# Kernel optimization log

Hardware: AMD Instinct MI355X
Metric: run time of the kernel (lower is better)

The kernel has to match this reference:

```python
import jax, jax.numpy as jnp
import numpy as np

EMBED_DIM = 768
NUM_HEADS = 12
HEAD_DIM = EMBED_DIM // NUM_HEADS
SCALE = HEAD_DIM ** -0.5
B, N = 8, 1024


def setup_inputs() -> dict:
    key = jax.random.key(0)
    ks = jax.random.split(key, 5)
    return {
        "x": jax.random.normal(ks[0], (B, N, EMBED_DIM), dtype=jnp.float32),
        "qkv_w": jax.random.normal(ks[1], (3 * EMBED_DIM, EMBED_DIM), dtype=jnp.float32) * 0.02,
        "qkv_b": jax.random.normal(ks[2], (3 * EMBED_DIM,), dtype=jnp.float32) * 0.02,
        "proj_w": jax.random.normal(ks[3], (EMBED_DIM, EMBED_DIM), dtype=jnp.float32) * 0.02,
        "proj_b": jax.random.normal(ks[4], (EMBED_DIM,), dtype=jnp.float32) * 0.02,
    }


def reference(x, qkv_w, qkv_b, proj_w, proj_b):
    b, n, c = x.shape
    h, hd = NUM_HEADS, HEAD_DIM
    # QKV projection: [b,n,3c]
    qkv = jnp.einsum("bnc,dc->bnd", x, qkv_w) + qkv_b
    qkv = qkv.reshape(b, n, 3, h, hd).transpose(2, 0, 3, 1, 4)  # [3,b,h,n,hd]
    q, k, v = qkv[0], qkv[1], qkv[2]
    # scaled dot-product attention (eager path; dropout is identity in eval)
    attn = jnp.einsum("bhqd,bhkd->bhqk", q, k) * SCALE
    attn = jax.nn.softmax(attn, axis=-1)
    out = jnp.einsum("bhqk,bhkd->bhqd", attn, v)  # [b,h,n,hd]
    out = out.transpose(0, 2, 1, 3).reshape(b, n, c)
    # output projection
    return jnp.einsum("bnc,dc->bnd", out, proj_w) + proj_b
```

## Files before the change

### kernel.cpp

```cpp
#include <hip/hip_runtime.h>
#include <hip/hip_bf16.h>

typedef __attribute__((ext_vector_type(4))) float f32x4;
typedef __attribute__((ext_vector_type(16))) float f32x16;
typedef __attribute__((ext_vector_type(8))) short short8;
typedef unsigned short u16;

#define MFMA(a, b, c) __builtin_amdgcn_mfma_f32_16x16x32_bf16((a), (b), (c), 0, 0, 0)
#define MFMA32(a, b, c) __builtin_amdgcn_mfma_f32_32x32x16_bf16((a), (b), (c), 0, 0, 0)

#define WAITVM_BAR(N) do {                                          \
    asm volatile("s_waitcnt vmcnt(" #N ")" ::: "memory");           \
    __builtin_amdgcn_s_barrier();                                   \
    __builtin_amdgcn_sched_barrier(0);                              \
} while (0)
#define BAR2() do {                                                 \
    __builtin_amdgcn_sched_barrier(0);                              \
    __builtin_amdgcn_s_barrier();                                   \
    __builtin_amdgcn_sched_barrier(0);                              \
} while (0)

static constexpr int EMBED = 768;
static constexpr int NH = 12;
static constexpr int HD = 64;
static constexpr int BATCH = 8;
static constexpr int SEQ = 1024;

__device__ __forceinline__ u16 f2bu(float f) {
    __hip_bfloat16 h = __float2bfloat16(f);
    u16 u; __builtin_memcpy(&u, &h, 2); return u;
}
__device__ __forceinline__ float exp2a(float x) {
    float r; asm("v_exp_f32 %0, %1" : "=v"(r) : "v"(x)); return r;
}
__device__ __forceinline__ unsigned cvt_pk_bf16(float lo, float hi) {
    unsigned r; asm("v_cvt_pk_bf16_f32 %0, %1, %2" : "=v"(r) : "v"(lo), "v"(hi)); return r;
}
__device__ __forceinline__ float max3f(float a, float b, float c) {
    return fmaxf(fmaxf(a, b), c);
}
__device__ __forceinline__ void swap32(unsigned& a, unsigned& b) {
    asm volatile("v_permlane32_swap_b32 %0, %1" : "+v"(a), "+v"(b));
}
__device__ __forceinline__ short8 mk8(unsigned w0, unsigned w1, unsigned w2, unsigned w3) {
    union { unsigned u[4]; short8 s; } c;
    c.u[0] = w0; c.u[1] = w1; c.u[2] = w2; c.u[3] = w3;
    return c.s;
}

__global__ void cvt_all_k(const float* __restrict__ x, const float* __restrict__ w1,
                          const float* __restrict__ w2,
                          u16* __restrict__ xb, u16* __restrict__ wb, u16* __restrict__ pw) {
    const int n1 = BATCH * SEQ * EMBED;
    const int n2 = 3 * EMBED * EMBED;
    const int n3 = EMBED * EMBED;
    int i = (blockIdx.x * blockDim.x + threadIdx.x) * 4;
    const float* src; u16* dst;
    if (i < n1)            { src = x  + i;             dst = xb + i; }
    else if (i < n1 + n2)  { src = w1 + (i - n1);      dst = wb + (i - n1); }
    else if (i < n1+n2+n3) { src = w2 + (i - n1 - n2); dst = pw + (i - n1 - n2); }
    else return;
    float4 v = *reinterpret_cast<const float4*>(src);
    ushort4 o;
    o.x = f2bu(v.x); o.y = f2bu(v.y); o.z = f2bu(v.z); o.w = f2bu(v.w);
    *reinterpret_cast<ushort4*>(dst) = o;
}

template <int EPI>
__global__ __launch_bounds__(256)
void gemm_bt_k(const u16* __restrict__ A, const u16* __restrict__ Bw,
               const float* __restrict__ bias,
               u16* __restrict__ q_out, u16* __restrict__ k_out,
               u16* __restrict__ vt_out, float* __restrict__ f_out)
{
    __shared__ __attribute__((aligned(16))) char smem[65536];
    const int tid  = threadIdx.x;
    const int wave = tid >> 6, lane = tid & 63;
    const int hi   = lane >> 4, l15 = lane & 15;
    const int wr   = wave >> 1, wc = wave & 1;
    const int bm   = blockIdx.x, bn = blockIdx.y;

    f32x4 acc[4][4] = {};

    const size_t arow0 = (size_t)bm * 128;
    const size_t brow0 = (size_t)bn * 128;

    auto stage = [&](int buf, int kt) {
        char* Ab = smem + buf * 32768;
        char* Bb = Ab + 16384;
#pragma unroll
        for (int c = 0; c < 4; ++c) {
            int ck   = c * 4 + wave;
            int p    = ck * 1024 + lane * 16;
            int row  = p >> 7;
            int pcol = (p & 127) ^ ((row & 7) << 4);
            const u16* srcA = A  + (arow0 + row) * EMBED + kt + (pcol >> 1);
            const u16* srcB = Bw + (brow0 + row) * EMBED + kt + (pcol >> 1);
            __builtin_amdgcn_global_load_lds((const __attribute__((address_space(1))) void*)srcA,
                                             (__attribute__((address_space(3))) void*)(Ab + ck * 1024), 16, 0, 0);
            __builtin_amdgcn_global_load_lds((const __attribute__((address_space(1))) void*)srcB,
                                             (__attribute__((address_space(3))) void*)(Bb + ck * 1024), 16, 0, 0);
        }
    };

    const int sw_l = (l15 & 7) << 4;
    int aoff[2], boff[2];
#pragma unroll
    for (int kk = 0; kk < 2; ++kk) {
        int col = (kk * 64 + hi * 16) ^ sw_l;
        aoff[kk] = (wr * 64 + l15) * 128 + col;
        boff[kk] = (wc * 64 + l15) * 128 + col;
    }

    auto comp = [&](int buf) {
#pragma unroll
        for (int kk = 0; kk < 2; ++kk) {
            short8 af[4], bf[4];
#pragma unroll
            for (int mi = 0; mi < 4; ++mi)
                af[mi] = *reinterpret_cast<const short8*>(smem + buf * 32768 + aoff[kk] + mi * 2048);
#pragma unroll
            for (int ni = 0; ni < 4; ++ni)
                bf[ni] = *reinterpret_cast<const short8*>(smem + buf * 32768 + 16384 + boff[kk] + ni * 2048);
#pragma unroll
            for (int mi = 0; mi < 4; ++mi)
#pragma unroll
                for (int ni = 0; ni < 4; ++ni)
                    acc[mi][ni] = MFMA(af[mi], bf[ni], acc[mi][ni]);
        }
    };

    stage(0, 0);
#pragma unroll
    for (int tt = 0; tt < 5; ++tt) {
        stage(1, (2 * tt + 1) * 64);
        WAITVM_BAR(8);
        comp(0);
        BAR2();
        stage(0, (2 * tt + 2) * 64);
        WAITVM_BAR(8);
        comp(1);
        BAR2();
    }
    stage(1, 11 * 64);
    WAITVM_BAR(8);
    comp(0);
    BAR2();
    WAITVM_BAR(0);
    comp(1);

#pragma unroll
    for (int mi = 0; mi < 4; ++mi) {
        int crow0 = bm * 128 + wr * 64 + mi * 16 + hi * 4;
#pragma unroll
        for (int ni = 0; ni < 4; ++ni) {
            int ccol = bn * 128 + wc * 64 + ni * 16 + l15;
            float bv = bias[ccol];
            if constexpr (EPI == 0) {
                int which = ccol / 768;
                int rem   = ccol - which * 768;
                int hh = rem >> 6, hd = rem & 63;
                int bb = crow0 >> 10, nn0 = crow0 & 1023;
                size_t bh = (size_t)(bb * NH + hh);
                if (which == 2) {
                    uint2 pk;
                    pk.x = cvt_pk_bf16(acc[mi][ni][0] + bv, acc[mi][ni][1] + bv);
                    pk.y = cvt_pk_bf16(acc[mi][ni][2] + bv, acc[mi][ni][3] + bv);
                    *reinterpret_cast<uint2*>(&vt_out[(bh * HD + hd) * SEQ + nn0]) = pk;
                } else if (which == 0) {
#pragma unroll
                    for (int r = 0; r < 4; ++r)
                        q_out[(bh * SEQ + nn0 + r) * HD + hd] =
                            f2bu((acc[mi][ni][r] + bv) * 0.18033688f);
                } else {
#pragma unroll
                    for (int r = 0; r < 4; ++r)
                        k_out[(bh * SEQ + nn0 + r) * HD + hd] = f2bu(acc[mi][ni][r] + bv);
                }
            } else {
#pragma unroll
                for (int r = 0; r < 4; ++r)
                    f_out[(size_t)(crow0 + r) * EMBED + ccol] = acc[mi][ni][r] + bv;
            }
        }
    }
}

__global__ __launch_bounds__(256, 3)
void attn_k(const u16* __restrict__ Q, const u16* __restrict__ K,
            const u16* __restrict__ Vt, u16* __restrict__ AO)
{
    __shared__ __attribute__((aligned(16))) u16 kv[3][8192];

    const int tid = threadIdx.x;
    const int w   = tid >> 6, lane = tid & 63;
    const int h   = lane >> 5, l31 = lane & 31;
    const int f   = blockIdx.x;
    const int xcd = f & 7, i = f >> 3;
    const int bh  = xcd * 12 + (i % 12);
    const int q0w = (i / 12) * 128 + w * 32;

    const u16* Qh = Q  + (size_t)bh * SEQ * HD;
    const u16* Kh = K  + (size_t)bh * SEQ * HD;
    const u16* Vh = Vt + (size_t)bh * HD * SEQ;

    short8 qf[4];
#pragma unroll
    for (int ds = 0; ds < 4; ++ds)
        qf[ds] = *reinterpret_cast<const short8*>(
            Qh + (size_t)(q0w + l31) * HD + ds * 16 + h * 8);
    __builtin_amdgcn_sched_barrier(0);

    const u16* sptr[4]; int doff[4]; int sadv[4];
#pragma unroll
    for (int c = 0; c < 4; ++c) {
        int ch = c * 4 + w;
        int mc = ch & 7;
        int p  = mc * 1024 + lane * 16;
        int row = p >> 7;
        int colb = (p & 127) ^ ((row & 7) << 4);
        if (ch < 8) { sptr[c] = Kh + (size_t)row * HD + (colb >> 1); sadv[c] = 64 * HD; doff[c] = mc * 512; }
        else        { sptr[c] = Vh + (size_t)row * SEQ + (colb >> 1); sadv[c] = 64;     doff[c] = 4096 + mc * 512; }
    }
    auto stage = [&](int buf, int t) {
#pragma unroll
        for (int c = 0; c < 4; ++c)
            __builtin_amdgcn_global_load_lds(
                (const __attribute__((address_space(1))) void*)(sptr[c] + (size_t)t * sadv[c]),
                (__attribute__((address_space(3))) void*)(&kv[buf][doff[c]]), 16, 0, 0);
    };

    stage(0, 0);
    stage(1, 1);

    const int sw_l = (l31 & 7) << 4;
    int koff[4];
#pragma unroll
    for (int ds = 0; ds < 4; ++ds)
        koff[ds] = l31 * 128 + ((ds * 32 + h * 16) ^ sw_l);

    union { unsigned u[4]; short8 s; } oc;
    oc.u[0] = oc.u[1] = oc.u[2] = oc.u[3] = 0x3F803F80u;
    const short8 ones8 = oc.s;

    f32x16 accO[2] = {};
    f32x16 lsum = {};
    float m = 8.f;

    auto tile = [&](int BC) {
        const char* base = (const char*)kv + BC * 16384;
        f32x16 st[2] = {{0}, {0}};
        __builtin_amdgcn_s_setprio(1);
#pragma unroll
        for (int mf = 0; mf < 2; ++mf)
#pragma unroll
            for (int ds = 0; ds < 4; ++ds) {
                short8 kf = *reinterpret_cast<const short8*>(base + mf * 4096 + koff[ds]);
                st[mf] = MFMA32(kf, qf[ds], st[mf]);
            }
        __builtin_amdgcn_s_setprio(0);

        float x0 = max3f(st[0][0],  st[0][1],  st[0][2]);
        float x1 = max3f(st[0][3],  st[0][4],  st[0][5]);
        float x2 = max3f(st[0][6],  st[0][7],  st[0][8]);
        float x3 = max3f(st[0][9],  st[0][10], st[0][11]);
        float x4 = max3f(st[0][12], st[0][13], st[0][14]);
        float x5 = max3f(st[0][15], st[1][0],  st[1][1]);
        float x6 = max3f(st[1][2],  st[1][3],  st[1][4]);
        float x7 = max3f(st[1][5],  st[1][6],  st[1][7]);
        float x8 = max3f(st[1][8],  st[1][9],  st[1][10]);
        float x9 = max3f(st[1][11], st[1][12], st[1][13]);
        float xa = fmaxf(st[1][14], st[1][15]);
        float tm = fmaxf(max3f(max3f(x0, x1, x2), max3f(x3, x4, x5), max3f(x6, x7, x8)),
                         max3f(x9, xa, -1e30f));
        tm = fmaxf(tm, __shfl_xor(tm, 32, 64));

        unsigned pkw[2][8];
#pragma unroll
        for (int mf = 0; mf < 2; ++mf)
#pragma unroll
            for (int p = 0; p < 8; ++p) {
                float e0 = exp2a(st[mf][2 * p]     - m);
                float e1 = exp2a(st[mf][2 * p + 1] - m);
                pkw[mf][p] = cvt_pk_bf16(e0, e1);
            }

        short8 pb[4];
#pragma unroll
        for (int ks = 0; ks < 4; ++ks) {
            int mf = ks >> 1, b4 = (ks & 1) * 4;
            unsigned E0 = pkw[mf][b4 + 0], E1 = pkw[mf][b4 + 1];
            unsigned D0 = pkw[mf][b4 + 2], D1 = pkw[mf][b4 + 3];
            swap32(E0, D0);
            swap32(E1, D1);
            pb[ks] = mk8(E0, E1, D0, D1);
        }

        __builtin_amdgcn_s_setprio(1);
#pragma unroll
        for (int ks = 0; ks < 4; ++ks)
            lsum = MFMA32(ones8, pb[ks], lsum);
#pragma unroll
        for (int df = 0; df < 2; ++df)
#pragma unroll
            for (int ks = 0; ks < 4; ++ks) {
                short8 vf = *reinterpret_cast<const short8*>(base + 8192 + df * 4096 + koff[ks]);
                accO[df] = MFMA32(vf, pb[ks], accO[df]);
            }
        __builtin_amdgcn_s_setprio(0);

        if (!__all(tm <= m + 8.f)) {
            float mn = fmaxf(m, tm);
            float s  = exp2a(m - mn);
            m = mn;
#pragma unroll
            for (int r = 0; r < 16; ++r) {
                accO[0][r] *= s; accO[1][r] *= s; lsum[r] *= s;
            }
        }
    };

    auto one = [&](int bc, int bs, int tn, bool ds) {
        asm volatile("s_waitcnt vmcnt(4)" ::: "memory");
        __builtin_amdgcn_s_barrier();
        __builtin_amdgcn_sched_barrier(0);
        if (ds) stage(bs, tn);
        tile(bc);
        __builtin_amdgcn_sched_barrier(0);
    };

    one(0, 2, 2, true);
    one(1, 0, 3, true);
    one(2, 1, 4, true);
    for (int g = 1; g < 5; ++g) {
        one(0, 2, 3 * g + 2, true);
        one(1, 0, 3 * g + 3, 3 * g + 3 <= 15);
        one(2, 1, 3 * g + 4, 3 * g + 4 <= 15);
    }
    asm volatile("s_waitcnt vmcnt(0)" ::: "memory");
    __builtin_amdgcn_s_barrier();
    __builtin_amdgcn_sched_barrier(0);
    tile(0);

    float linv = 1.f / lsum[0];
    const int bb = bh / NH, hh = bh - bb * NH;
    size_t rowb = ((size_t)bb * SEQ + q0w + l31) * EMBED + hh * HD;
#pragma unroll
    for (int df = 0; df < 2; ++df)
#pragma unroll
        for (int g = 0; g < 4; ++g) {
            float o0 = accO[df][4 * g + 0] * linv;
            float o1 = accO[df][4 * g + 1] * linv;
            float o2 = accO[df][4 * g + 2] * linv;
            float o3 = accO[df][4 * g + 3] * linv;
            uint2 pk;
            pk.x = cvt_pk_bf16(o0, o1);
            pk.y = cvt_pk_bf16(o2, o3);
            *reinterpret_cast<uint2*>(&AO[rowb + df * 32 + 8 * g + 4 * h]) = pk;
        }
}

extern "C" void kernel_launch(void* const* d_in, const int* in_sizes, int n_in,
                              void* d_out, int out_size, void* d_ws, size_t ws_size,
                              hipStream_t stream)
{
    const float* x      = (const float*)d_in[0];
    const float* qkv_w  = (const float*)d_in[1];
    const float* qkv_b  = (const float*)d_in[2];
    const float* proj_w = (const float*)d_in[3];
    const float* proj_b = (const float*)d_in[4];
    float* out = (float*)d_out;

    char* ws = (char*)d_ws;
    u16* xb  = (u16*)(ws);
    u16* wb  = (u16*)(ws + 12582912);
    u16* pw  = (u16*)(ws + 16121856);
    u16* qb  = (u16*)(ws + 17301504);
    u16* kb  = (u16*)(ws + 29884416);
    u16* vt  = (u16*)(ws + 42467328);
    u16* ao  = (u16*)(ws + 55050240);

    cvt_all_k<<<8448, 256, 0, stream>>>(x, qkv_w, proj_w, xb, wb, pw);

    gemm_bt_k<0><<<dim3(64, 18), 256, 0, stream>>>(xb, wb, qkv_b, qb, kb, vt, nullptr);
    attn_k<<<768, 256, 0, stream>>>(qb, kb, vt, ao);
    gemm_bt_k<1><<<dim3(64, 6), 256, 0, stream>>>(ao, pw, proj_b, nullptr, nullptr, nullptr, out);
}
```

Before: 102.6 us.

## Widen GEMM tile to 128x256 with triple-buffered LDS pipeline

The shared bf16 GEMM now computes a 128x256 output tile per block instead of 128x128, doubling each wave's accumulators and B fragments so every A fragment loaded from LDS feeds twice as many MFMAs. LDS staging moves from double to triple buffering with a single barrier per k-step, and the global-to-LDS source pointers are precomputed once outside the loop. The grids halve to 64x9 and 64x3 blocks. This raises register and LDS use (144KB per block), which limits occupancy to one block per CU, and the proj GEMM launches only 192 blocks.

```diff
diff --git a/kernel.cpp b/kernel.cpp
--- a/kernel.cpp
+++ b/kernel.cpp
@@ -11,11 +11,6 @@
 
 #define WAITVM_BAR(N) do {                                          \
     asm volatile("s_waitcnt vmcnt(" #N ")" ::: "memory");           \
-    __builtin_amdgcn_s_barrier();                                   \
-    __builtin_amdgcn_sched_barrier(0);                              \
-} while (0)
-#define BAR2() do {                                                 \
-    __builtin_amdgcn_sched_barrier(0);                              \
     __builtin_amdgcn_s_barrier();                                   \
     __builtin_amdgcn_sched_barrier(0);                              \
 } while (0)
@@ -73,34 +68,43 @@
                u16* __restrict__ q_out, u16* __restrict__ k_out,
                u16* __restrict__ vt_out, float* __restrict__ f_out)
 {
-    __shared__ __attribute__((aligned(16))) char smem[65536];
+    __shared__ __attribute__((aligned(16))) char smem[147456];
     const int tid  = threadIdx.x;
     const int wave = tid >> 6, lane = tid & 63;
     const int hi   = lane >> 4, l15 = lane & 15;
     const int wr   = wave >> 1, wc = wave & 1;
     const int bm   = blockIdx.x, bn = blockIdx.y;
 
-    f32x4 acc[4][4] = {};
+    f32x4 acc[4][8] = {};
 
     const size_t arow0 = (size_t)bm * 128;
-    const size_t brow0 = (size_t)bn * 128;
-
-    auto stage = [&](int buf, int kt) {
-        char* Ab = smem + buf * 32768;
-        char* Bb = Ab + 16384;
-#pragma unroll
-        for (int c = 0; c < 4; ++c) {
-            int ck   = c * 4 + wave;
-            int p    = ck * 1024 + lane * 16;
+    const size_t brow0 = (size_t)bn * 256;
+
+    const u16* sptr[12]; int dofs[12];
+#pragma unroll
+    for (int c = 0; c < 12; ++c) {
+        int ch = c * 4 + wave;
+        if (ch < 16) {
+            int p    = ch * 1024 + lane * 16;
             int row  = p >> 7;
             int pcol = (p & 127) ^ ((row & 7) << 4);
-            const u16* srcA = A  + (arow0 + row) * EMBED + kt + (pcol >> 1);
-            const u16* srcB = Bw + (brow0 + row) * EMBED + kt + (pcol >> 1);
-            __builtin_amdgcn_global_load_lds((const __attribute__((address_space(1))) void*)srcA,
-                                             (__attribute__((address_space(3))) void*)(Ab + ck * 1024), 16, 0, 0);
-            __builtin_amdgcn_global_load_lds((const __attribute__((address_space(1))) void*)srcB,
-                                             (__attribute__((address_space(3))) void*)(Bb + ck * 1024), 16, 0, 0);
-        }
+            sptr[c] = A + (arow0 + row) * EMBED + (pcol >> 1);
+            dofs[c] = ch * 1024;
+        } else {
+            int p    = (ch - 16) * 1024 + lane * 16;
+            int row  = p >> 7;
+            int pcol = (p & 127) ^ ((row & 7) << 4);
+            sptr[c] = Bw + (brow0 + row) * EMBED + (pcol >> 1);
+            dofs[c] = 16384 + (ch - 16) * 1024;
+        }
+    }
+    auto stage = [&](int buf, int kt) {
+        char* base = smem + buf * 49152;
+#pragma unroll
+        for (int c = 0; c < 12; ++c)
+            __builtin_amdgcn_global_load_lds(
+                (const __attribute__((address_space(1))) void*)(sptr[c] + kt),
+                (__attribute__((address_space(3))) void*)(base + dofs[c]), 16, 0, 0);
     };
 
     const int sw_l = (l15 & 7) << 4;
@@ -109,52 +113,57 @@
     for (int kk = 0; kk < 2; ++kk) {
         int col = (kk * 64 + hi * 16) ^ sw_l;
         aoff[kk] = (wr * 64 + l15) * 128 + col;
-        boff[kk] = (wc * 64 + l15) * 128 + col;
+        boff[kk] = 16384 + (wc * 128 + l15) * 128 + col;
     }
 
     auto comp = [&](int buf) {
+        const char* base = smem + buf * 49152;
 #pragma unroll
         for (int kk = 0; kk < 2; ++kk) {
-            short8 af[4], bf[4];
+            short8 af[4], bf[8];
 #pragma unroll
             for (int mi = 0; mi < 4; ++mi)
-                af[mi] = *reinterpret_cast<const short8*>(smem + buf * 32768 + aoff[kk] + mi * 2048);
-#pragma unroll
-            for (int ni = 0; ni < 4; ++ni)
-                bf[ni] = *reinterpret_cast<const short8*>(smem + buf * 32768 + 16384 + boff[kk] + ni * 2048);
+                af[mi] = *reinterpret_cast<const short8*>(base + aoff[kk] + mi * 2048);
+#pragma unroll
+            for (int ni = 0; ni < 8; ++ni)
+                bf[ni] = *reinterpret_cast<const short8*>(base + boff[kk] + ni * 2048);
 #pragma unroll
             for (int mi = 0; mi < 4; ++mi)
 #pragma unroll
-                for (int ni = 0; ni < 4; ++ni)
+                for (int ni = 0; ni < 8; ++ni)
                     acc[mi][ni] = MFMA(af[mi], bf[ni], acc[mi][ni]);
         }
     };
 
+    auto one = [&](int bc, int bs, int tn, bool ds) {
+        asm volatile("s_waitcnt vmcnt(12)" ::: "memory");
+        __builtin_amdgcn_s_barrier();
+        __builtin_amdgcn_sched_barrier(0);
+        if (ds) stage(bs, tn * 64);
+        comp(bc);
+        __builtin_amdgcn_sched_barrier(0);
+    };
+
     stage(0, 0);
-#pragma unroll
-    for (int tt = 0; tt < 5; ++tt) {
-        stage(1, (2 * tt + 1) * 64);
-        WAITVM_BAR(8);
-        comp(0);
-        BAR2();
-        stage(0, (2 * tt + 2) * 64);
-        WAITVM_BAR(8);
-        comp(1);
-        BAR2();
-    }
-    stage(1, 11 * 64);
-    WAITVM_BAR(8);
-    comp(0);
-    BAR2();
-    WAITVM_BAR(0);
-    comp(1);
+    stage(1, 64);
+    for (int g = 0; g < 3; ++g) {
+        one(0, 2, 3 * g + 2, true);
+        one(1, 0, 3 * g + 3, true);
+        one(2, 1, 3 * g + 4, true);
+    }
+    one(0, 2, 11, true);
+    one(1, 0, 0, false);
+    asm volatile("s_waitcnt vmcnt(0)" ::: "memory");
+    __builtin_amdgcn_s_barrier();
+    __builtin_amdgcn_sched_barrier(0);
+    comp(2);
 
 #pragma unroll
     for (int mi = 0; mi < 4; ++mi) {
         int crow0 = bm * 128 + wr * 64 + mi * 16 + hi * 4;
 #pragma unroll
-        for (int ni = 0; ni < 4; ++ni) {
-            int ccol = bn * 128 + wc * 64 + ni * 16 + l15;
+        for (int ni = 0; ni < 8; ++ni) {
+            int ccol = bn * 256 + wc * 128 + ni * 16 + l15;
             float bv = bias[ccol];
             if constexpr (EPI == 0) {
                 int which = ccol / 768;
@@ -382,7 +391,7 @@
 
     cvt_all_k<<<8448, 256, 0, stream>>>(x, qkv_w, proj_w, xb, wb, pw);
 
-    gemm_bt_k<0><<<dim3(64, 18), 256, 0, stream>>>(xb, wb, qkv_b, qb, kb, vt, nullptr);
+    gemm_bt_k<0><<<dim3(64, 9), 256, 0, stream>>>(xb, wb, qkv_b, qb, kb, vt, nullptr);
     attn_k<<<768, 256, 0, stream>>>(qb, kb, vt, ao);
-    gemm_bt_k<1><<<dim3(64, 6), 256, 0, stream>>>(ao, pw, proj_b, nullptr, nullptr, nullptr, out);
-}
+    gemm_bt_k<1><<<dim3(64, 3), 256, 0, stream>>>(ao, pw, proj_b, nullptr, nullptr, nullptr, out);
+}
```

Result: slower. 123.1 us (+19.9%).
